# Kernel tuning notes

Measured on AMD Instinct MI355X. Metric: run time of the kernel, lower is better.

## Reference

```python
import jax, jax.numpy as jnp
import numpy as np

B, N, L, S, D, H = 16, 8, 64, 32, 256, 128  # 2*H == D required by the module


def _lstm_dir(seq, Wih, Whh, bih, bhh):
    # seq: [T, B, D] -> hidden states [T, B, H]; PyTorch gate order i,f,g,o
    Hd = Whh.shape[1]
    b = seq.shape[1]

    def step(carry, xt):
        h, c = carry
        gates = xt @ Wih.T + h @ Whh.T + bih + bhh  # [B, 4H]
        i, f, g, o = jnp.split(gates, 4, axis=-1)
        c = jax.nn.sigmoid(f) * c + jax.nn.sigmoid(i) * jnp.tanh(g)
        h = jax.nn.sigmoid(o) * jnp.tanh(c)
        return (h, c), h

    init = (jnp.zeros((b, Hd), seq.dtype), jnp.zeros((b, Hd), seq.dtype))
    _, hs = jax.lax.scan(step, init, seq)
    return hs


def setup_inputs() -> dict:
    key = jax.random.key(0)
    ks = jax.random.split(key, 16)
    sc = 1.0 / np.sqrt(D)
    sch = 1.0 / np.sqrt(H)
    inp = {
        "x": jax.random.normal(ks[0], (B, N, L, D), jnp.float32),
        "s": jax.random.normal(ks[1], (B, S, D), jnp.float32),
        # co-attention params (Linear(dim,dim,bias=False) stored [out,in])
        "W": jax.random.normal(ks[2], (D, D), jnp.float32) * sc,
        "U": jax.random.normal(ks[3], (D, D), jnp.float32) * sc,
        "v": jax.random.normal(ks[4], (D,), jnp.float32) * sc,
        # BiLSTM params, forward and backward directions
        "Wih_f": jax.random.normal(ks[5], (4 * H, D), jnp.float32) * sch,
        "Whh_f": jax.random.normal(ks[6], (4 * H, H), jnp.float32) * sch,
        "bih_f": jax.random.normal(ks[7], (4 * H,), jnp.float32) * sch,
        "bhh_f": jax.random.normal(ks[8], (4 * H,), jnp.float32) * sch,
        "Wih_b": jax.random.normal(ks[9], (4 * H, D), jnp.float32) * sch,
        "Whh_b": jax.random.normal(ks[10], (4 * H, H), jnp.float32) * sch,
        "bih_b": jax.random.normal(ks[11], (4 * H,), jnp.float32) * sch,
        "bhh_b": jax.random.normal(ks[12], (4 * H,), jnp.float32) * sch,
        # self-attention params (Linear(D,D) with bias, Linear(D,1) no bias)
        "saW": jax.random.normal(ks[13], (D, D), jnp.float32) * sc,
        "sab": jax.random.normal(ks[14], (D,), jnp.float32) * sc,
        "sav": jax.random.normal(ks[15], (D,), jnp.float32) * sc,
    }
    return inp


def reference(x, s, W, U, v, Wih_f, Whh_f, bih_f, bhh_f,
              Wih_b, Whh_b, bih_b, bhh_b, saW, sab, sav):
    # ---- CoAttention (vectorized over B, N, S) ----
    Wx = jnp.einsum('bnld,ed->bnle', x, W)          # [B,N,L,D]
    Us = jnp.einsum('bsd,ed->bse', s, U)            # [B,S,D]
    # additive attention: tanh(Wx + Us) . v  -> scores over L
    e = jnp.tanh(Wx[:, :, None, :, :] + Us[:, None, :, None, :])  # [B,N,S,L,D]
    scores = jnp.einsum('bnsld,d->bnsl', e, v)      # [B,N,S,L]
    a = jax.nn.softmax(scores, axis=-1)             # softmax over L (dim=0 of [L,B] in torch)
    sr = jnp.einsum('bnsl,bnld->bnsd', a, x)        # [B,N,S,D]
    sr = sr.mean(axis=2)                            # [B,N,D]

    # ---- BiLSTM over the N axis ----
    u = jnp.swapaxes(sr, 0, 1)                      # [N,B,D]
    hf = _lstm_dir(u, Wih_f, Whh_f, bih_f, bhh_f)   # [N,B,H]
    hb = _lstm_dir(u[::-1], Wih_b, Whh_b, bih_b, bhh_b)[::-1]
    c = jnp.swapaxes(jnp.concatenate([hf, hb], axis=-1), 0, 1)  # [B,N,2H]

    # ---- Self-attention pooling ----
    att = jnp.tanh(c @ saW.T + sab) @ sav           # [B,N]
    att = jax.nn.softmax(att, axis=1)
    g = jnp.einsum('bn,bnd->bd', att, c)            # [B,2H]
    return g
```

## Files before the change

kernel.cpp:

```cpp
#include <hip/hip_runtime.h>
#include <cstddef>

#define Bsz 16
#define Nn  8
#define Ll  64
#define Ss  32
#define Dd  256
#define Hh  128

#define LOG2E 1.4426950408889634f

__device__ __forceinline__ float rcp_f(float x)  { return __builtin_amdgcn_rcpf(x); }
__device__ __forceinline__ float exp2_f(float x) { return __builtin_amdgcn_exp2f(x); }

__device__ __forceinline__ float fast_tanh(float x) {
    return 1.0f - 2.0f * rcp_f(exp2_f(x * (2.0f * LOG2E)) + 1.0f);
}
__device__ __forceinline__ float fast_sigmoid(float x) {
    return rcp_f(1.0f + exp2_f(-x * LOG2E));
}
__device__ __forceinline__ float wave_sum(float x) {
#pragma unroll
    for (int off = 32; off > 0; off >>= 1) x += __shfl_xor(x, off, 64);
    return x;
}
__device__ __forceinline__ float wave_max(float x) {
#pragma unroll
    for (int off = 32; off > 0; off >>= 1) x = fmaxf(x, __shfl_xor(x, off, 64));
    return x;
}

__global__ __launch_bounds__(256) void transpose_all(
    const float* __restrict__ W, const float* __restrict__ U, const float* __restrict__ saW,
    const float* __restrict__ Wih_f, const float* __restrict__ Wih_b,
    float* __restrict__ WT, float* __restrict__ UT, float* __restrict__ saWT,
    float* __restrict__ WihT)
{
    __shared__ float ts[64][65];
    int blk = blockIdx.x, tid = threadIdx.x;
    const float* src; float* dst; int C, ldo, coff, t;
    if (blk < 16)      { src = W;     dst = WT;   C = 256; ldo = 256;  coff = 0;   t = blk;      }
    else if (blk < 32) { src = U;     dst = UT;   C = 256; ldo = 256;  coff = 0;   t = blk - 16; }
    else if (blk < 48) { src = saW;   dst = saWT; C = 256; ldo = 256;  coff = 0;   t = blk - 32; }
    else if (blk < 80) { src = Wih_f; dst = WihT; C = 256; ldo = 1024; coff = 0;   t = blk - 48; }
    else               { src = Wih_b; dst = WihT; C = 256; ldo = 1024; coff = 512; t = blk - 80; }
    int r0 = (t >> 2) * 64, c0 = (t & 3) * 64;
    int f = tid & 15, r = tid >> 4;
#pragma unroll
    for (int p = 0; p < 4; ++p) {
        int rr = r + 16 * p;
        float4 tv = *(const float4*)&src[(size_t)(r0 + rr) * C + c0 + 4 * f];
        ts[rr][4 * f + 0] = tv.x; ts[rr][4 * f + 1] = tv.y;
        ts[rr][4 * f + 2] = tv.z; ts[rr][4 * f + 3] = tv.w;
    }
    __syncthreads();
#pragma unroll
    for (int p = 0; p < 4; ++p) {
        int oc = (tid >> 4) + 16 * p;
        float4 o;
        o.x = ts[4 * f + 0][oc]; o.y = ts[4 * f + 1][oc];
        o.z = ts[4 * f + 2][oc]; o.w = ts[4 * f + 3][oc];
        *(float4*)&dst[(size_t)(c0 + oc) * ldo + coff + r0 + 4 * f] = o;
    }
}

__global__ __launch_bounds__(256) void gemm_nt(const float* __restrict__ A,
                                               const float* __restrict__ BT,
                                               float* __restrict__ C, int M, int N, int K)
{
    __shared__ float As[64][44];
    __shared__ float Bs[32][68];
    const int tid = threadIdx.x;
    const int tx = tid & 15, ty = tid >> 4;
    const int m0 = blockIdx.y * 64, n0 = blockIdx.x * 64;
    const int ka = tid & 31, ma = tid >> 5;
    const int nb = tid & 63, kb = tid >> 6;
    float acc[4][4] = {};
    for (int kc = 0; kc < K; kc += 32) {
#pragma unroll
        for (int r = 0; r < 8; ++r)
            As[ma + r * 8][ka] = A[(size_t)(m0 + ma + r * 8) * K + kc + ka];
#pragma unroll
        for (int r = 0; r < 8; ++r)
            Bs[kb + r * 4][nb] = BT[(size_t)(kc + kb + r * 4) * N + n0 + nb];
        __syncthreads();
#pragma unroll
        for (int kk = 0; kk < 32; kk += 4) {
            float ar[4][4], br[4][4];
#pragma unroll
            for (int i = 0; i < 4; ++i) {
                float4 t = *(const float4*)&As[ty * 4 + i][kk];
                ar[i][0] = t.x; ar[i][1] = t.y; ar[i][2] = t.z; ar[i][3] = t.w;
            }
#pragma unroll
            for (int q = 0; q < 4; ++q) {
                float4 t = *(const float4*)&Bs[kk + q][tx * 4];
                br[q][0] = t.x; br[q][1] = t.y; br[q][2] = t.z; br[q][3] = t.w;
            }
#pragma unroll
            for (int q = 0; q < 4; ++q)
#pragma unroll
                for (int i = 0; i < 4; ++i)
#pragma unroll
                    for (int j = 0; j < 4; ++j)
                        acc[i][j] = fmaf(ar[i][q], br[q][j], acc[i][j]);
        }
        __syncthreads();
    }
#pragma unroll
    for (int i = 0; i < 4; ++i) {
        float4 o; o.x = acc[i][0]; o.y = acc[i][1]; o.z = acc[i][2]; o.w = acc[i][3];
        *(float4*)&C[(size_t)(m0 + ty * 4 + i) * N + n0 + tx * 4] = o;
    }
}

__global__ __launch_bounds__(512, 1) void scores_kernel(const float* __restrict__ Wx,
                                                        const float* __restrict__ Us,
                                                        const float* __restrict__ v,
                                                        float* __restrict__ a_buf)
{
    __shared__ float wx[64][260];
    __shared__ float us[16][256];
    __shared__ float sc[16][64];
    const int bid = blockIdx.x;
    const int bn = bid >> 1, sh = bid & 1;
    const int b = bn >> 3;
    const int tid = threadIdx.x;
    const int lane = tid & 63, w = tid >> 6;
    {
        const float* wxg = Wx + (size_t)bn * (Ll * Dd);
        int c = tid & 63, r0 = tid >> 6;
#pragma unroll
        for (int p = 0; p < 8; ++p) {
            int r = r0 + p * 8;
            float4 t = *(const float4*)&wxg[r * 256 + c * 4];
            *(float4*)&wx[r][c * 4] = t;
        }
        const float* usg = Us + ((size_t)b * Ss + sh * 16) * 256;
#pragma unroll
        for (int p = 0; p < 2; ++p) {
            int r = r0 + p * 8;
            float4 t = *(const float4*)&usg[r * 256 + c * 4];
            *(float4*)&us[r][c * 4] = t;
        }
    }
    __syncthreads();
    const float C2 = 2.0f * LOG2E;
    float4 v4 = *(const float4*)&v[lane * 4];
    float vsum = wave_sum(v4.x + v4.y + v4.z + v4.w);
    const int s0 = w * 2, s1 = s0 + 1;
    float4 ua = *(const float4*)&us[s0][lane * 4];
    float4 ub = *(const float4*)&us[s1][lane * 4];
    ua.x *= C2; ua.y *= C2; ua.z *= C2; ua.w *= C2;
    ub.x *= C2; ub.y *= C2; ub.z *= C2; ub.w *= C2;
    for (int l = 0; l < 64; ++l) {
        float4 wv = *(const float4*)&wx[l][lane * 4];
        float cx = wv.x * C2, cy = wv.y * C2, cz = wv.z * C2, cw = wv.w * C2;
        float a0 =       v4.x * rcp_f(exp2_f(cx + ua.x) + 1.0f);
        a0 = fmaf(v4.y, rcp_f(exp2_f(cy + ua.y) + 1.0f), a0);
        a0 = fmaf(v4.z, rcp_f(exp2_f(cz + ua.z) + 1.0f), a0);
        a0 = fmaf(v4.w, rcp_f(exp2_f(cw + ua.w) + 1.0f), a0);
        float a1 =       v4.x * rcp_f(exp2_f(cx + ub.x) + 1.0f);
        a1 = fmaf(v4.y, rcp_f(exp2_f(cy + ub.y) + 1.0f), a1);
        a1 = fmaf(v4.z, rcp_f(exp2_f(cz + ub.z) + 1.0f), a1);
        a1 = fmaf(v4.w, rcp_f(exp2_f(cw + ub.w) + 1.0f), a1);
        a0 = wave_sum(a0);
        a1 = wave_sum(a1);
        if (lane == 0) { sc[s0][l] = vsum - 2.0f * a0; sc[s1][l] = vsum - 2.0f * a1; }
    }
    __syncthreads();
    float sv0 = sc[s0][lane], sv1 = sc[s1][lane];
    float e0 = exp2_f((sv0 - wave_max(sv0)) * LOG2E);
    float e1 = exp2_f((sv1 - wave_max(sv1)) * LOG2E);
    float i0 = rcp_f(wave_sum(e0));
    float i1 = rcp_f(wave_sum(e1));
    float* ab = a_buf + ((size_t)bn * Ss + sh * 16) * 64;
    ab[s0 * 64 + lane] = e0 * i0;
    ab[s1 * 64 + lane] = e1 * i1;
}

__global__ __launch_bounds__(256) void sr_kernel(const float* __restrict__ a_buf,
                                                 const float* __restrict__ x,
                                                 float* __restrict__ sr_nb)
{
    int bn = blockIdx.x;
    int b = bn >> 3, n = bn & 7;
    int tid = threadIdx.x;
    __shared__ float abar[64];
    __shared__ float red[4][64];
    {
        int l = tid & 63, sg = tid >> 6;
        float p = 0.f;
        for (int s = sg * 8; s < sg * 8 + 8; ++s)
            p += a_buf[((size_t)bn * 32 + s) * 64 + l];
        red[sg][l] = p;
        __syncthreads();
        if (tid < 64)
            abar[tid] = (red[0][tid] + red[1][tid] + red[2][tid] + red[3][tid]) * (1.0f / 32.0f);
        __syncthreads();
    }
    float acc = 0.f;
    const float* xp = x + (size_t)bn * Ll * Dd;
    for (int l = 0; l < Ll; ++l)
        acc = fmaf(abar[l], xp[l * Dd + tid], acc);
    sr_nb[((size_t)n * Bsz + b) * Dd + tid] = acc;
}

__global__ __launch_bounds__(512) void lstm_kernel(const float* __restrict__ gx,
                                                   const float* __restrict__ Whh_f,
                                                   const float* __restrict__ Whh_b,
                                                   const float* __restrict__ bih_f, const float* __restrict__ bhh_f,
                                                   const float* __restrict__ bih_b, const float* __restrict__ bhh_b,
                                                   float* __restrict__ h_out)
{
    int blk = blockIdx.x;
    int dir = blk >> 4, b = blk & 15;
    int g = threadIdx.x;
    const float* wr = ((dir == 0) ? Whh_f : Whh_b) + (size_t)g * 128;
    float4 w4[32];
#pragma unroll
    for (int k = 0; k < 32; ++k) w4[k] = ((const float4*)wr)[k];
    float bias = (dir == 0) ? (bih_f[g] + bhh_f[g]) : (bih_b[g] + bhh_b[g]);
    __shared__ float h[128], c[128], gb[512];
    if (g < 128) { h[g] = 0.f; c[g] = 0.f; }
    __syncthreads();
    for (int t = 0; t < Nn; ++t) {
        int n = (dir == 0) ? t : (Nn - 1 - t);
        float a0 = gx[((size_t)(n * Bsz + b)) * 1024 + dir * 512 + g] + bias;
        float a1 = 0.f, a2 = 0.f, a3 = 0.f;
#pragma unroll
        for (int k = 0; k < 32; ++k) {
            float4 hv = *(const float4*)&h[k * 4];
            a0 = fmaf(w4[k].x, hv.x, a0);
            a1 = fmaf(w4[k].y, hv.y, a1);
            a2 = fmaf(w4[k].z, hv.z, a2);
            a3 = fmaf(w4[k].w, hv.w, a3);
        }
        float pre = (a0 + a1) + (a2 + a3);
        float act = (g < 256 || g >= 384) ? fast_sigmoid(pre) : fast_tanh(pre);
        gb[g] = act;
        __syncthreads();
        if (g < 128) {
            float i_ = gb[g], f_ = gb[128 + g], g_ = gb[256 + g], o_ = gb[384 + g];
            float cn = fmaf(f_, c[g], i_ * g_);
            float hn = o_ * fast_tanh(cn);
            c[g] = cn; h[g] = hn;
            h_out[(((size_t)dir * Nn + n) * Bsz + b) * Hh + g] = hn;
        }
        __syncthreads();
    }
}

__global__ __launch_bounds__(256) void attpool_kernel(const float* __restrict__ hbuf,
                                                      const float* __restrict__ saWT,
                                                      const float* __restrict__ sab,
                                                      const float* __restrict__ sav,
                                                      float* __restrict__ out)
{
    int b = blockIdx.x;
    int e = threadIdx.x;
    __shared__ float cvec[8][260];
    __shared__ float part[8][4];
#pragma unroll
    for (int n = 0; n < 8; ++n) {
        float val = (e < 128) ? hbuf[((size_t)(0 * Nn + n) * Bsz + b) * Hh + e]
                              : hbuf[((size_t)(1 * Nn + n) * Bsz + b) * Hh + (e - 128)];
        cvec[n][e] = val;
    }
    __syncthreads();
    float acc[8];
    float b0 = sab[e];
#pragma unroll
    for (int n = 0; n < 8; ++n) acc[n] = b0;
    for (int dq = 0; dq < 64; ++dq) {
        float w0 = saWT[(dq * 4 + 0) * 256 + e];
        float w1 = saWT[(dq * 4 + 1) * 256 + e];
        float w2 = saWT[(dq * 4 + 2) * 256 + e];
        float w3 = saWT[(dq * 4 + 3) * 256 + e];
#pragma unroll
        for (int n = 0; n < 8; ++n) {
            float4 cv = *(const float4*)&cvec[n][dq * 4];
            acc[n] = fmaf(w0, cv.x, acc[n]);
            acc[n] = fmaf(w1, cv.y, acc[n]);
            acc[n] = fmaf(w2, cv.z, acc[n]);
            acc[n] = fmaf(w3, cv.w, acc[n]);
        }
    }
    int w = e >> 6, lane = e & 63;
    float se = sav[e];
#pragma unroll
    for (int n = 0; n < 8; ++n) {
        float t = fast_tanh(acc[n]) * se;
        t = wave_sum(t);
        if (lane == 0) part[n][w] = t;
    }
    __syncthreads();
    float av[8], mx = -1e30f;
#pragma unroll
    for (int n = 0; n < 8; ++n) {
        av[n] = part[n][0] + part[n][1] + part[n][2] + part[n][3];
        mx = fmaxf(mx, av[n]);
    }
    float sum = 0.f;
#pragma unroll
    for (int n = 0; n < 8; ++n) { av[n] = exp2_f((av[n] - mx) * LOG2E); sum += av[n]; }
    float inv = rcp_f(sum);
    float acco = 0.f;
#pragma unroll
    for (int n = 0; n < 8; ++n) acco = fmaf(av[n], cvec[n][e], acco);
    out[b * 256 + e] = acco * inv;
}

extern "C" void kernel_launch(void* const* d_in, const int* in_sizes, int n_in,
                              void* d_out, int out_size, void* d_ws, size_t ws_size,
                              hipStream_t stream) {
    const float* x     = (const float*)d_in[0];
    const float* s     = (const float*)d_in[1];
    const float* W     = (const float*)d_in[2];
    const float* U     = (const float*)d_in[3];
    const float* v     = (const float*)d_in[4];
    const float* Wih_f = (const float*)d_in[5];
    const float* Whh_f = (const float*)d_in[6];
    const float* bih_f = (const float*)d_in[7];
    const float* bhh_f = (const float*)d_in[8];
    const float* Wih_b = (const float*)d_in[9];
    const float* Whh_b = (const float*)d_in[10];
    const float* bih_b = (const float*)d_in[11];
    const float* bhh_b = (const float*)d_in[12];
    const float* saW   = (const float*)d_in[13];
    const float* sab   = (const float*)d_in[14];
    const float* sav   = (const float*)d_in[15];
    float* out = (float*)d_out;
    float* ws  = (float*)d_ws;

    float* WT    = ws;
    float* UT    = WT + 65536;
    float* saWT  = UT + 65536;
    float* WihT  = saWT + 65536;
    float* Wx    = WihT + 262144;
    float* Us    = Wx + 2097152;
    float* a_buf = Us + 131072;
    float* sr_nb = a_buf + 262144;
    float* gx    = sr_nb + 32768;
    float* hbuf  = gx + 131072;

    hipLaunchKernelGGL(transpose_all, dim3(112), dim3(256), 0, stream,
                       W, U, saW, Wih_f, Wih_b, WT, UT, saWT, WihT);
    hipLaunchKernelGGL(gemm_nt, dim3(4, 128), dim3(256), 0, stream, x, WT, Wx, 8192, 256, 256);
    hipLaunchKernelGGL(gemm_nt, dim3(4, 8), dim3(256), 0, stream, s, UT, Us, 512, 256, 256);
    hipLaunchKernelGGL(scores_kernel, dim3(256), dim3(512), 0, stream, Wx, Us, v, a_buf);
    hipLaunchKernelGGL(sr_kernel, dim3(128), dim3(256), 0, stream, a_buf, x, sr_nb);
    hipLaunchKernelGGL(gemm_nt, dim3(16, 2), dim3(256), 0, stream, sr_nb, WihT, gx, 128, 1024, 256);
    hipLaunchKernelGGL(lstm_kernel, dim3(32), dim3(512), 0, stream,
                       gx, Whh_f, Whh_b, bih_f, bhh_f, bih_b, bhh_b, hbuf);
    hipLaunchKernelGGL(attpool_kernel, dim3(16), dim3(256), 0, stream, hbuf, saWT, sab, sav, out);
}
```

Before: 200.9 us.

## Drop weight transpose kernel; use NT-layout GEMM tiles and merge GEMM launches

Removes the transpose_all kernel by rewriting the GEMM to read row-major weights directly, with 128x64 tiles and K-contiguous float4 loads for both operands. The x·W and s·U GEMMs are merged into one launch, and the gx GEMM now reads Wih_f/Wih_b directly. The attention-pool kernel now reads saW rows rather than the transposed copy. The 2*log2e scaling in scores_kernel is folded into the shared-memory staging, and the sr loop is unrolled. This cuts two launches and a pass over the weights, at the cost of uncoalesced per-thread row reads of saW and a GEMM that processes 128 rows per block.

```diff
diff --git a/kernel.cpp b/kernel.cpp
--- a/kernel.cpp
+++ b/kernel.cpp
@@ -30,88 +30,94 @@
     return x;
 }
 
-__global__ __launch_bounds__(256) void transpose_all(
-    const float* __restrict__ W, const float* __restrict__ U, const float* __restrict__ saW,
-    const float* __restrict__ Wih_f, const float* __restrict__ Wih_b,
-    float* __restrict__ WT, float* __restrict__ UT, float* __restrict__ saWT,
-    float* __restrict__ WihT)
-{
-    __shared__ float ts[64][65];
-    int blk = blockIdx.x, tid = threadIdx.x;
-    const float* src; float* dst; int C, ldo, coff, t;
-    if (blk < 16)      { src = W;     dst = WT;   C = 256; ldo = 256;  coff = 0;   t = blk;      }
-    else if (blk < 32) { src = U;     dst = UT;   C = 256; ldo = 256;  coff = 0;   t = blk - 16; }
-    else if (blk < 48) { src = saW;   dst = saWT; C = 256; ldo = 256;  coff = 0;   t = blk - 32; }
-    else if (blk < 80) { src = Wih_f; dst = WihT; C = 256; ldo = 1024; coff = 0;   t = blk - 48; }
-    else               { src = Wih_b; dst = WihT; C = 256; ldo = 1024; coff = 512; t = blk - 80; }
-    int r0 = (t >> 2) * 64, c0 = (t & 3) * 64;
-    int f = tid & 15, r = tid >> 4;
-#pragma unroll
-    for (int p = 0; p < 4; ++p) {
-        int rr = r + 16 * p;
-        float4 tv = *(const float4*)&src[(size_t)(r0 + rr) * C + c0 + 4 * f];
-        ts[rr][4 * f + 0] = tv.x; ts[rr][4 * f + 1] = tv.y;
-        ts[rr][4 * f + 2] = tv.z; ts[rr][4 * f + 3] = tv.w;
-    }
-    __syncthreads();
-#pragma unroll
-    for (int p = 0; p < 4; ++p) {
-        int oc = (tid >> 4) + 16 * p;
-        float4 o;
-        o.x = ts[4 * f + 0][oc]; o.y = ts[4 * f + 1][oc];
-        o.z = ts[4 * f + 2][oc]; o.w = ts[4 * f + 3][oc];
-        *(float4*)&dst[(size_t)(c0 + oc) * ldo + coff + r0 + 4 * f] = o;
-    }
-}
-
-__global__ __launch_bounds__(256) void gemm_nt(const float* __restrict__ A,
-                                               const float* __restrict__ BT,
-                                               float* __restrict__ C, int M, int N, int K)
-{
-    __shared__ float As[64][44];
-    __shared__ float Bs[32][68];
+__device__ __forceinline__ void gemm_tile_128x64(const float* __restrict__ A,
+                                                 const float* __restrict__ B,
+                                                 float* __restrict__ C,
+                                                 int ldc,
+                                                 float (* __restrict__ As)[44],
+                                                 float (* __restrict__ Bs)[44])
+{
     const int tid = threadIdx.x;
-    const int tx = tid & 15, ty = tid >> 4;
-    const int m0 = blockIdx.y * 64, n0 = blockIdx.x * 64;
-    const int ka = tid & 31, ma = tid >> 5;
-    const int nb = tid & 63, kb = tid >> 6;
-    float acc[4][4] = {};
-    for (int kc = 0; kc < K; kc += 32) {
-#pragma unroll
-        for (int r = 0; r < 8; ++r)
-            As[ma + r * 8][ka] = A[(size_t)(m0 + ma + r * 8) * K + kc + ka];
-#pragma unroll
-        for (int r = 0; r < 8; ++r)
-            Bs[kb + r * 4][nb] = BT[(size_t)(kc + kb + r * 4) * N + n0 + nb];
+    const int kq = tid & 7;
+    const int mr = tid >> 3;
+    const int tx = tid & 15;
+    const int ty = tid >> 4;
+    float acc[8][4] = {};
+    for (int kc = 0; kc < 256; kc += 32) {
+#pragma unroll
+        for (int p = 0; p < 4; ++p) {
+            float4 t = *(const float4*)&A[(size_t)(mr + 32 * p) * 256 + kc + kq * 4];
+            *(float4*)&As[mr + 32 * p][kq * 4] = t;
+        }
+#pragma unroll
+        for (int p = 0; p < 2; ++p) {
+            float4 t = *(const float4*)&B[(size_t)(mr + 32 * p) * 256 + kc + kq * 4];
+            *(float4*)&Bs[mr + 32 * p][kq * 4] = t;
+        }
         __syncthreads();
 #pragma unroll
         for (int kk = 0; kk < 32; kk += 4) {
-            float ar[4][4], br[4][4];
-#pragma unroll
-            for (int i = 0; i < 4; ++i) {
-                float4 t = *(const float4*)&As[ty * 4 + i][kk];
-                ar[i][0] = t.x; ar[i][1] = t.y; ar[i][2] = t.z; ar[i][3] = t.w;
+            float4 br[4];
+#pragma unroll
+            for (int j = 0; j < 4; ++j) br[j] = *(const float4*)&Bs[tx + 16 * j][kk];
+#pragma unroll
+            for (int i = 0; i < 8; ++i) {
+                float4 a = *(const float4*)&As[ty + 16 * i][kk];
+#pragma unroll
+                for (int j = 0; j < 4; ++j) {
+                    acc[i][j] = fmaf(a.x, br[j].x, acc[i][j]);
+                    acc[i][j] = fmaf(a.y, br[j].y, acc[i][j]);
+                    acc[i][j] = fmaf(a.z, br[j].z, acc[i][j]);
+                    acc[i][j] = fmaf(a.w, br[j].w, acc[i][j]);
+                }
             }
-#pragma unroll
-            for (int q = 0; q < 4; ++q) {
-                float4 t = *(const float4*)&Bs[kk + q][tx * 4];
-                br[q][0] = t.x; br[q][1] = t.y; br[q][2] = t.z; br[q][3] = t.w;
-            }
-#pragma unroll
-            for (int q = 0; q < 4; ++q)
-#pragma unroll
-                for (int i = 0; i < 4; ++i)
-#pragma unroll
-                    for (int j = 0; j < 4; ++j)
-                        acc[i][j] = fmaf(ar[i][q], br[q][j], acc[i][j]);
-        }
-        __syncthreads();
-    }
-#pragma unroll
-    for (int i = 0; i < 4; ++i) {
-        float4 o; o.x = acc[i][0]; o.y = acc[i][1]; o.z = acc[i][2]; o.w = acc[i][3];
-        *(float4*)&C[(size_t)(m0 + ty * 4 + i) * N + n0 + tx * 4] = o;
-    }
+        }
+        __syncthreads();
+    }
+#pragma unroll
+    for (int i = 0; i < 8; ++i)
+#pragma unroll
+        for (int j = 0; j < 4; ++j)
+            C[(size_t)(ty + 16 * i) * ldc + tx + 16 * j] = acc[i][j];
+}
+
+__global__ __launch_bounds__(256) void gemm_stage1(const float* __restrict__ x,
+                                                   const float* __restrict__ s,
+                                                   const float* __restrict__ W,
+                                                   const float* __restrict__ U,
+                                                   float* __restrict__ Wx,
+                                                   float* __restrict__ Us)
+{
+    __shared__ float As[128][44];
+    __shared__ float Bs[64][44];
+    int blk = blockIdx.x;
+    const float *Ap, *Bp; float* Cp;
+    if (blk < 256) {
+        int my = blk >> 2, nx = blk & 3;
+        Ap = x + (size_t)my * 128 * 256;
+        Bp = W + (size_t)nx * 64 * 256;
+        Cp = Wx + (size_t)my * 128 * 256 + nx * 64;
+    } else {
+        int b2 = blk - 256;
+        int my = b2 >> 2, nx = b2 & 3;
+        Ap = s + (size_t)my * 128 * 256;
+        Bp = U + (size_t)nx * 64 * 256;
+        Cp = Us + (size_t)my * 128 * 256 + nx * 64;
+    }
+    gemm_tile_128x64(Ap, Bp, Cp, 256, As, Bs);
+}
+
+__global__ __launch_bounds__(256) void gemm_gx(const float* __restrict__ sr,
+                                               const float* __restrict__ Wf,
+                                               const float* __restrict__ Wb,
+                                               float* __restrict__ gx)
+{
+    __shared__ float As[128][44];
+    __shared__ float Bs[64][44];
+    int blk = blockIdx.x;
+    int dir = blk >> 3, nx = blk & 7;
+    const float* Bp = (dir ? Wb : Wf) + (size_t)nx * 64 * 256;
+    gemm_tile_128x64(sr, Bp, gx + dir * 512 + nx * 64, 1024, As, Bs);
 }
 
 __global__ __launch_bounds__(512, 1) void scores_kernel(const float* __restrict__ Wx,
@@ -127,6 +133,7 @@
     const int b = bn >> 3;
     const int tid = threadIdx.x;
     const int lane = tid & 63, w = tid >> 6;
+    const float C2 = 2.0f * LOG2E;
     {
         const float* wxg = Wx + (size_t)bn * (Ll * Dd);
         int c = tid & 63, r0 = tid >> 6;
@@ -134,6 +141,7 @@
         for (int p = 0; p < 8; ++p) {
             int r = r0 + p * 8;
             float4 t = *(const float4*)&wxg[r * 256 + c * 4];
+            t.x *= C2; t.y *= C2; t.z *= C2; t.w *= C2;
             *(float4*)&wx[r][c * 4] = t;
         }
         const float* usg = Us + ((size_t)b * Ss + sh * 16) * 256;
@@ -141,29 +149,26 @@
         for (int p = 0; p < 2; ++p) {
             int r = r0 + p * 8;
             float4 t = *(const float4*)&usg[r * 256 + c * 4];
+            t.x *= C2; t.y *= C2; t.z *= C2; t.w *= C2;
             *(float4*)&us[r][c * 4] = t;
         }
     }
     __syncthreads();
-    const float C2 = 2.0f * LOG2E;
     float4 v4 = *(const float4*)&v[lane * 4];
     float vsum = wave_sum(v4.x + v4.y + v4.z + v4.w);
     const int s0 = w * 2, s1 = s0 + 1;
     float4 ua = *(const float4*)&us[s0][lane * 4];
     float4 ub = *(const float4*)&us[s1][lane * 4];
-    ua.x *= C2; ua.y *= C2; ua.z *= C2; ua.w *= C2;
-    ub.x *= C2; ub.y *= C2; ub.z *= C2; ub.w *= C2;
     for (int l = 0; l < 64; ++l) {
         float4 wv = *(const float4*)&wx[l][lane * 4];
-        float cx = wv.x * C2, cy = wv.y * C2, cz = wv.z * C2, cw = wv.w * C2;
-        float a0 =       v4.x * rcp_f(exp2_f(cx + ua.x) + 1.0f);
-        a0 = fmaf(v4.y, rcp_f(exp2_f(cy + ua.y) + 1.0f), a0);
-        a0 = fmaf(v4.z, rcp_f(exp2_f(cz + ua.z) + 1.0f), a0);
-        a0 = fmaf(v4.w, rcp_f(exp2_f(cw + ua.w) + 1.0f), a0);
-        float a1 =       v4.x * rcp_f(exp2_f(cx + ub.x) + 1.0f);
-        a1 = fmaf(v4.y, rcp_f(exp2_f(cy + ub.y) + 1.0f), a1);
-        a1 = fmaf(v4.z, rcp_f(exp2_f(cz + ub.z) + 1.0f), a1);
-        a1 = fmaf(v4.w, rcp_f(exp2_f(cw + ub.w) + 1.0f), a1);
+        float a0 =       v4.x * rcp_f(exp2_f(wv.x + ua.x) + 1.0f);
+        a0 = fmaf(v4.y, rcp_f(exp2_f(wv.y + ua.y) + 1.0f), a0);
+        a0 = fmaf(v4.z, rcp_f(exp2_f(wv.z + ua.z) + 1.0f), a0);
+        a0 = fmaf(v4.w, rcp_f(exp2_f(wv.w + ua.w) + 1.0f), a0);
+        float a1 =       v4.x * rcp_f(exp2_f(wv.x + ub.x) + 1.0f);
+        a1 = fmaf(v4.y, rcp_f(exp2_f(wv.y + ub.y) + 1.0f), a1);
+        a1 = fmaf(v4.z, rcp_f(exp2_f(wv.z + ub.z) + 1.0f), a1);
+        a1 = fmaf(v4.w, rcp_f(exp2_f(wv.w + ub.w) + 1.0f), a1);
         a0 = wave_sum(a0);
         a1 = wave_sum(a1);
         if (lane == 0) { sc[s0][l] = vsum - 2.0f * a0; sc[s1][l] = vsum - 2.0f * a1; }
@@ -201,6 +206,7 @@
     }
     float acc = 0.f;
     const float* xp = x + (size_t)bn * Ll * Dd;
+#pragma unroll 8
     for (int l = 0; l < Ll; ++l)
         acc = fmaf(abar[l], xp[l * Dd + tid], acc);
     sr_nb[((size_t)n * Bsz + b) * Dd + tid] = acc;
@@ -252,7 +258,7 @@
 }
 
 __global__ __launch_bounds__(256) void attpool_kernel(const float* __restrict__ hbuf,
-                                                      const float* __restrict__ saWT,
+                                                      const float* __restrict__ saW,
                                                       const float* __restrict__ sab,
                                                       const float* __restrict__ sav,
                                                       float* __restrict__ out)
@@ -262,28 +268,30 @@
     __shared__ float cvec[8][260];
     __shared__ float part[8][4];
 #pragma unroll
-    for (int n = 0; n < 8; ++n) {
-        float val = (e < 128) ? hbuf[((size_t)(0 * Nn + n) * Bsz + b) * Hh + e]
-                              : hbuf[((size_t)(1 * Nn + n) * Bsz + b) * Hh + (e - 128)];
-        cvec[n][e] = val;
-    }
-    __syncthreads();
+    for (int n = 0; n < 8; ++n)
+        cvec[n][e] = (e < 128) ? hbuf[((size_t)n * Bsz + b) * Hh + e]
+                               : hbuf[((size_t)(Nn + n) * Bsz + b) * Hh + (e - 128)];
+    __syncthreads();
+    const float* wrow = saW + (size_t)e * 256;
     float acc[8];
     float b0 = sab[e];
 #pragma unroll
     for (int n = 0; n < 8; ++n) acc[n] = b0;
-    for (int dq = 0; dq < 64; ++dq) {
-        float w0 = saWT[(dq * 4 + 0) * 256 + e];
-        float w1 = saWT[(dq * 4 + 1) * 256 + e];
-        float w2 = saWT[(dq * 4 + 2) * 256 + e];
-        float w3 = saWT[(dq * 4 + 3) * 256 + e];
-#pragma unroll
-        for (int n = 0; n < 8; ++n) {
-            float4 cv = *(const float4*)&cvec[n][dq * 4];
-            acc[n] = fmaf(w0, cv.x, acc[n]);
-            acc[n] = fmaf(w1, cv.y, acc[n]);
-            acc[n] = fmaf(w2, cv.z, acc[n]);
-            acc[n] = fmaf(w3, cv.w, acc[n]);
+#pragma unroll 2
+    for (int dq0 = 0; dq0 < 8; ++dq0) {
+        float4 wq[8];
+#pragma unroll
+        for (int q = 0; q < 8; ++q) wq[q] = *(const float4*)&wrow[dq0 * 32 + q * 4];
+#pragma unroll
+        for (int q = 0; q < 8; ++q) {
+#pragma unroll
+            for (int n = 0; n < 8; ++n) {
+                float4 cv = *(const float4*)&cvec[n][dq0 * 32 + q * 4];
+                acc[n] = fmaf(wq[q].x, cv.x, acc[n]);
+                acc[n] = fmaf(wq[q].y, cv.y, acc[n]);
+                acc[n] = fmaf(wq[q].z, cv.z, acc[n]);
+                acc[n] = fmaf(wq[q].w, cv.w, acc[n]);
+            }
         }
     }
     int w = e >> 6, lane = e & 63;
@@ -333,25 +341,18 @@
     float* out = (float*)d_out;
     float* ws  = (float*)d_ws;
 
-    float* WT    = ws;
-    float* UT    = WT + 65536;
-    float* saWT  = UT + 65536;
-    float* WihT  = saWT + 65536;
-    float* Wx    = WihT + 262144;
+    float* Wx    = ws;
     float* Us    = Wx + 2097152;
     float* a_buf = Us + 131072;
     float* sr_nb = a_buf + 262144;
     float* gx    = sr_nb + 32768;
     float* hbuf  = gx + 131072;
 
-    hipLaunchKernelGGL(transpose_all, dim3(112), dim3(256), 0, stream,
-                       W, U, saW, Wih_f, Wih_b, WT, UT, saWT, WihT);
-    hipLaunchKernelGGL(gemm_nt, dim3(4, 128), dim3(256), 0, stream, x, WT, Wx, 8192, 256, 256);
-    hipLaunchKernelGGL(gemm_nt, dim3(4, 8), dim3(256), 0, stream, s, UT, Us, 512, 256, 256);
+    hipLaunchKernelGGL(gemm_stage1, dim3(272), dim3(256), 0, stream, x, s, W, U, Wx, Us);
     hipLaunchKernelGGL(scores_kernel, dim3(256), dim3(512), 0, stream, Wx, Us, v, a_buf);
     hipLaunchKernelGGL(sr_kernel, dim3(128), dim3(256), 0, stream, a_buf, x, sr_nb);
-    hipLaunchKernelGGL(gemm_nt, dim3(16, 2), dim3(256), 0, stream, sr_nb, WihT, gx, 128, 1024, 256);
+    hipLaunchKernelGGL(gemm_gx, dim3(16), dim3(256), 0, stream, sr_nb, Wih_f, Wih_b, gx);
     hipLaunchKernelGGL(lstm_kernel, dim3(32), dim3(512), 0, stream,
                        gx, Whh_f, Whh_b, bih_f, bhh_f, bih_b, bhh_b, hbuf);
-    hipLaunchKernelGGL(attpool_kernel, dim3(16), dim3(256), 0, stream, hbuf, saWT, sab, sav, out);
-}
+    hipLaunchKernelGGL(attpool_kernel, dim3(16), dim3(256), 0, stream, hbuf, saW, sab, sav, out);
+}
```

Result: slower. 213.2 us (+6.1%).
